# Optimization experiments

Measured on AMD Instinct MI355X. Metric: run time of the kernel, lower is better.

## Reference

```python
import jax, jax.numpy as jnp
import numpy as np


def setup_inputs() -> dict:
    key = jax.random.key(0)
    k1, k2, k3 = jax.random.split(key, 3)
    B, K, C, H, W = 8, 8, 256, 64, 64
    return {
        "IR_features": jax.random.normal(k1, (B, K, C, H, W), dtype=jnp.float32),
        "CR_features": jax.random.normal(k2, (B, K, C, H, W), dtype=jnp.float32),
        "CT_feature": jax.random.normal(k3, (B, C, H, W), dtype=jnp.float32),
    }


def reference(IR_features, CR_features, CT_feature):
    # sim: [B, K, C, 1, 1] = <CT, CR>_{HW} / ||CR||_{HW}
    dot = jnp.sum(CT_feature[:, None] * CR_features, axis=(3, 4), keepdims=True)
    norm = jnp.sqrt(jnp.sum(CR_features ** 2, axis=(3, 4), keepdims=True))
    sim = dot / norm
    weights = jax.nn.softmax(sim * 2.0, axis=1)  # softmax over K styles
    # style feature: weighted sum over K -> [B, C, H, W]
    style_feature = jnp.sum(IR_features * weights, axis=1)
    return style_feature
```

## Files before the change

### kernel.cpp

```cpp
#include <hip/hip_runtime.h>
#include <math.h>

#define B_DIM 8
#define K_DIM 8
#define C_DIM 256
#define HW4   1024

__global__ __launch_bounds__(1024, 8)
void dfs_mixer_fused(const float4* __restrict__ IR,
                     const float4* __restrict__ CR,
                     const float4* __restrict__ CT,
                     float4* __restrict__ out)
{
    const int bid  = blockIdx.x;
    const int b    = bid >> 8;
    const int c    = bid & 255;
    const int t    = threadIdx.x;
    const int wave = t >> 6;
    const int lane = t & 63;

    const int ct_base = bid * HW4;

    const int k  = wave >> 1;
    const int li = ((wave & 1) << 6) | lane;
    const int cr_base = (b * (K_DIM * C_DIM) + k * C_DIM + c) * HW4;

    float d = 0.f, s = 0.f;
#pragma unroll
    for (int i = 0; i < 8; ++i) {
        const int off = li + i * 128;
        float4 ctv = CT[ct_base + off];
        float4 crv = CR[cr_base + off];
        d = fmaf(ctv.x, crv.x, d); d = fmaf(ctv.y, crv.y, d);
        d = fmaf(ctv.z, crv.z, d); d = fmaf(ctv.w, crv.w, d);
        s = fmaf(crv.x, crv.x, s); s = fmaf(crv.y, crv.y, s);
        s = fmaf(crv.z, crv.z, s); s = fmaf(crv.w, crv.w, s);
    }

#pragma unroll
    for (int off = 32; off >= 1; off >>= 1) {
        d += __shfl_xor(d, off, 64);
        s += __shfl_xor(s, off, 64);
    }

    __shared__ float red_d[16];
    __shared__ float red_s[16];
    __shared__ float simbuf[K_DIM];
    __shared__ float wts[K_DIM];
    if (lane == 0) { red_d[wave] = d; red_s[wave] = s; }
    __syncthreads();

    if (t < K_DIM) {
        float dd = red_d[2 * t] + red_d[2 * t + 1];
        float ss = red_s[2 * t] + red_s[2 * t + 1];
        simbuf[t] = 2.0f * dd / sqrtf(ss);
    }
    __syncthreads();

    if (t < K_DIM) {
        float m = -1e30f;
#pragma unroll
        for (int j = 0; j < K_DIM; ++j) m = fmaxf(m, simbuf[j]);
        float sum = 0.f;
#pragma unroll
        for (int j = 0; j < K_DIM; ++j) sum += expf(simbuf[j] - m);
        wts[t] = expf(simbuf[t] - m) / sum;
    }
    __syncthreads();

    float w[K_DIM];
#pragma unroll
    for (int j = 0; j < K_DIM; ++j) w[j] = wts[j];

    const int plane0 = (b * (K_DIM * C_DIM) + c) * HW4 + t;
    float4 acc = make_float4(0.f, 0.f, 0.f, 0.f);
#pragma unroll
    for (int j = 0; j < K_DIM; ++j) {
        float4 v = IR[plane0 + j * (C_DIM * HW4)];
        acc.x = fmaf(w[j], v.x, acc.x);
        acc.y = fmaf(w[j], v.y, acc.y);
        acc.z = fmaf(w[j], v.z, acc.z);
        acc.w = fmaf(w[j], v.w, acc.w);
    }
    out[ct_base + t] = acc;
}

extern "C" void kernel_launch(void* const* d_in, const int* in_sizes, int n_in,
                              void* d_out, int out_size, void* d_ws, size_t ws_size,
                              hipStream_t stream) {
    const float4* IR = (const float4*)d_in[0];
    const float4* CR = (const float4*)d_in[1];
    const float4* CT = (const float4*)d_in[2];
    float4* out      = (float4*)d_out;

    dfs_mixer_fused<<<B_DIM * C_DIM, 1024, 0, stream>>>(IR, CR, CT, out);
}
```

Measured before the change: 532.2 us.

## Split fused mixer into separate similarity and mixing kernels

Replaces the single fused kernel with two launches. The first computes one similarity value per (b,c,k) using 256-thread blocks and writes it to workspace. The second computes the softmax per (b,c) and does the weighted sum over IR with 256 threads, each handling four float4 outputs with all eight loads issued together. The aim is to remove the block-wide barriers that stalled the big 1024-thread blocks and to get more parallelism and more loads in flight, at the cost of an extra launch and a small round trip through global memory. CT is now re-read once per k.

```diff
diff --git a/kernel.cpp b/kernel.cpp
--- a/kernel.cpp
+++ b/kernel.cpp
@@ -6,35 +6,34 @@
 #define C_DIM 256
 #define HW4   1024
 
-__global__ __launch_bounds__(1024, 8)
-void dfs_mixer_fused(const float4* __restrict__ IR,
-                     const float4* __restrict__ CR,
-                     const float4* __restrict__ CT,
-                     float4* __restrict__ out)
+__global__ __launch_bounds__(256, 4)
+void dfs_sim(const float4* __restrict__ CR,
+             const float4* __restrict__ CT,
+             float* __restrict__ sims)
 {
-    const int bid  = blockIdx.x;
-    const int b    = bid >> 8;
-    const int c    = bid & 255;
-    const int t    = threadIdx.x;
-    const int wave = t >> 6;
-    const int lane = t & 63;
+    const int bid = blockIdx.x;
+    const int k   = bid & 7;
+    const int bc  = bid >> 3;
+    const int b   = bc >> 8;
+    const int c   = bc & 255;
+    const int t   = threadIdx.x;
 
-    const int ct_base = bid * HW4;
+    const float4* __restrict__ ctp = CT + (size_t)bc * HW4;
+    const float4* __restrict__ crp = CR + (size_t)((b * K_DIM + k) * C_DIM + c) * HW4;
 
-    const int k  = wave >> 1;
-    const int li = ((wave & 1) << 6) | lane;
-    const int cr_base = (b * (K_DIM * C_DIM) + k * C_DIM + c) * HW4;
-
+    float4 a[4], r[4];
+#pragma unroll
+    for (int i = 0; i < 4; ++i) {
+        a[i] = ctp[t + i * 256];
+        r[i] = crp[t + i * 256];
+    }
     float d = 0.f, s = 0.f;
 #pragma unroll
-    for (int i = 0; i < 8; ++i) {
-        const int off = li + i * 128;
-        float4 ctv = CT[ct_base + off];
-        float4 crv = CR[cr_base + off];
-        d = fmaf(ctv.x, crv.x, d); d = fmaf(ctv.y, crv.y, d);
-        d = fmaf(ctv.z, crv.z, d); d = fmaf(ctv.w, crv.w, d);
-        s = fmaf(crv.x, crv.x, s); s = fmaf(crv.y, crv.y, s);
-        s = fmaf(crv.z, crv.z, s); s = fmaf(crv.w, crv.w, s);
+    for (int i = 0; i < 4; ++i) {
+        d = fmaf(a[i].x, r[i].x, d); d = fmaf(a[i].y, r[i].y, d);
+        d = fmaf(a[i].z, r[i].z, d); d = fmaf(a[i].w, r[i].w, d);
+        s = fmaf(r[i].x, r[i].x, s); s = fmaf(r[i].y, r[i].y, s);
+        s = fmaf(r[i].z, r[i].z, s); s = fmaf(r[i].w, r[i].w, s);
     }
 
 #pragma unroll
@@ -42,47 +41,61 @@
         d += __shfl_xor(d, off, 64);
         s += __shfl_xor(s, off, 64);
     }
+    __shared__ float rd[4], rs[4];
+    const int wave = t >> 6, lane = t & 63;
+    if (lane == 0) { rd[wave] = d; rs[wave] = s; }
+    __syncthreads();
+    if (t == 0) {
+        const float dd = rd[0] + rd[1] + rd[2] + rd[3];
+        const float ss = rs[0] + rs[1] + rs[2] + rs[3];
+        sims[bid] = 2.0f * dd / sqrtf(ss);
+    }
+}
 
-    __shared__ float red_d[16];
-    __shared__ float red_s[16];
-    __shared__ float simbuf[K_DIM];
-    __shared__ float wts[K_DIM];
-    if (lane == 0) { red_d[wave] = d; red_s[wave] = s; }
-    __syncthreads();
+__global__ __launch_bounds__(256, 4)
+void dfs_mix(const float4* __restrict__ IR,
+             const float* __restrict__ sims,
+             float4* __restrict__ out)
+{
+    const int bc = blockIdx.x;
+    const int b  = bc >> 8;
+    const int c  = bc & 255;
+    const int t  = threadIdx.x;
 
-    if (t < K_DIM) {
-        float dd = red_d[2 * t] + red_d[2 * t + 1];
-        float ss = red_s[2 * t] + red_s[2 * t + 1];
-        simbuf[t] = 2.0f * dd / sqrtf(ss);
+    float si[K_DIM];
+#pragma unroll
+    for (int j = 0; j < K_DIM; ++j) si[j] = sims[bc * K_DIM + j];
+    float m = si[0];
+#pragma unroll
+    for (int j = 1; j < K_DIM; ++j) m = fmaxf(m, si[j]);
+    float w[K_DIM];
+    float sum = 0.f;
+#pragma unroll
+    for (int j = 0; j < K_DIM; ++j) { w[j] = expf(si[j] - m); sum += w[j]; }
+    const float inv = 1.0f / sum;
+#pragma unroll
+    for (int j = 0; j < K_DIM; ++j) w[j] *= inv;
+
+    const size_t plane0  = (size_t)(b * K_DIM * C_DIM + c) * HW4;
+    const size_t kstride = (size_t)C_DIM * HW4;
+    const size_t obase   = (size_t)bc * HW4;
+
+#pragma unroll
+    for (int i = 0; i < 4; ++i) {
+        const int off = t + i * 256;
+        float4 v[K_DIM];
+#pragma unroll
+        for (int j = 0; j < K_DIM; ++j) v[j] = IR[plane0 + j * kstride + off];
+        float4 acc = make_float4(0.f, 0.f, 0.f, 0.f);
+#pragma unroll
+        for (int j = 0; j < K_DIM; ++j) {
+            acc.x = fmaf(w[j], v[j].x, acc.x);
+            acc.y = fmaf(w[j], v[j].y, acc.y);
+            acc.z = fmaf(w[j], v[j].z, acc.z);
+            acc.w = fmaf(w[j], v[j].w, acc.w);
+        }
+        out[obase + off] = acc;
     }
-    __syncthreads();
-
-    if (t < K_DIM) {
-        float m = -1e30f;
-#pragma unroll
-        for (int j = 0; j < K_DIM; ++j) m = fmaxf(m, simbuf[j]);
-        float sum = 0.f;
-#pragma unroll
-        for (int j = 0; j < K_DIM; ++j) sum += expf(simbuf[j] - m);
-        wts[t] = expf(simbuf[t] - m) / sum;
-    }
-    __syncthreads();
-
-    float w[K_DIM];
-#pragma unroll
-    for (int j = 0; j < K_DIM; ++j) w[j] = wts[j];
-
-    const int plane0 = (b * (K_DIM * C_DIM) + c) * HW4 + t;
-    float4 acc = make_float4(0.f, 0.f, 0.f, 0.f);
-#pragma unroll
-    for (int j = 0; j < K_DIM; ++j) {
-        float4 v = IR[plane0 + j * (C_DIM * HW4)];
-        acc.x = fmaf(w[j], v.x, acc.x);
-        acc.y = fmaf(w[j], v.y, acc.y);
-        acc.z = fmaf(w[j], v.z, acc.z);
-        acc.w = fmaf(w[j], v.w, acc.w);
-    }
-    out[ct_base + t] = acc;
 }
 
 extern "C" void kernel_launch(void* const* d_in, const int* in_sizes, int n_in,
@@ -92,6 +105,8 @@
     const float4* CR = (const float4*)d_in[1];
     const float4* CT = (const float4*)d_in[2];
     float4* out      = (float4*)d_out;
+    float* sims      = (float*)d_ws;
 
-    dfs_mixer_fused<<<B_DIM * C_DIM, 1024, 0, stream>>>(IR, CR, CT, out);
+    dfs_sim<<<B_DIM * C_DIM * K_DIM, 256, 0, stream>>>(CR, CT, sims);
+    dfs_mix<<<B_DIM * C_DIM, 256, 0, stream>>>(IR, sims, out);
 }
```

Result: no change. 530.4 us (-0.3%).
